# Performance work log

Hardware: AMD Instinct MI355X
Metric: run time of the kernel (lower is better)

## Reference

```python
import jax, jax.numpy as jnp
import numpy as np

TOP_K = 2
NUM_EXPERTS = 8
D_MODEL = 1024


def setup_inputs() -> dict:
    key = jax.random.key(0)
    kx, kw, kb = jax.random.split(key, 3)
    x = jax.random.normal(kx, (8, 4096, D_MODEL), dtype=jnp.float32)
    bound = 1.0 / np.sqrt(D_MODEL)
    W = jax.random.uniform(kw, (NUM_EXPERTS, D_MODEL), dtype=jnp.float32, minval=-bound, maxval=bound)
    b = jax.random.uniform(kb, (NUM_EXPERTS,), dtype=jnp.float32, minval=-bound, maxval=bound)
    return {"x": x, "W": W, "b": b}


def reference(x, W, b):
    # logits: [B, S, E]
    logits = jnp.einsum('bsd,ed->bse', x, W) + b
    values, indices = jax.lax.top_k(logits, TOP_K)  # [B,S,K]
    # softmax over a tensor that is -inf everywhere except top-k positions
    # == softmax over the top-k values, scattered back; non-selected experts get 0.
    topk_w = jax.nn.softmax(values, axis=-1)  # [B,S,K]
    one_hot = jax.nn.one_hot(indices, NUM_EXPERTS, dtype=logits.dtype)  # [B,S,K,E]
    weights = jnp.einsum('bsk,bske->bse', topk_w, one_hot)
    return weights, indices
```

## Files before the change

kernel.cpp:

```cpp
#include <hip/hip_runtime.h>
#include <math.h>

#define D_MODEL 1024
#define NUM_EXPERTS 8
#define TOP_K 2
#define TOKENS_PER_WAVE 4
#define WAVES_PER_BLOCK 4
#define TOKENS_PER_BLOCK (TOKENS_PER_WAVE * WAVES_PER_BLOCK)

__global__ __launch_bounds__(256) void gating_kernel(
    const float* __restrict__ x, const float* __restrict__ W,
    const float* __restrict__ b, float* __restrict__ out_w,
    float* __restrict__ out_idx, int n_tokens)
{
    __shared__ float Wlds[NUM_EXPERTS * D_MODEL];

    {
        const float4* Wg = (const float4*)W;
        float4* Ws = (float4*)Wlds;
        const int tid = threadIdx.x;
#pragma unroll
        for (int i = 0; i < (NUM_EXPERTS * D_MODEL / 4) / 256; ++i)
            Ws[tid + i * 256] = Wg[tid + i * 256];
    }
    __syncthreads();

    const int wave = threadIdx.x >> 6;
    const int lane = threadIdx.x & 63;
    const int token0 = (blockIdx.x * WAVES_PER_BLOCK + wave) * TOKENS_PER_WAVE;
    if (token0 >= n_tokens) return;

    float acc[TOKENS_PER_WAVE][NUM_EXPERTS];
#pragma unroll
    for (int t = 0; t < TOKENS_PER_WAVE; ++t)
#pragma unroll
        for (int e = 0; e < NUM_EXPERTS; ++e) acc[t][e] = 0.f;

#pragma unroll
    for (int j = 0; j < D_MODEL / 256; ++j) {
        float4 xv[TOKENS_PER_WAVE];
#pragma unroll
        for (int t = 0; t < TOKENS_PER_WAVE; ++t)
            xv[t] = *(const float4*)(x + (size_t)(token0 + t) * D_MODEL + j * 256 + lane * 4);
#pragma unroll
        for (int e = 0; e < NUM_EXPERTS; ++e) {
            float4 wv = *(const float4*)(Wlds + e * D_MODEL + j * 256 + lane * 4);
#pragma unroll
            for (int t = 0; t < TOKENS_PER_WAVE; ++t) {
                acc[t][e] += xv[t].x * wv.x + xv[t].y * wv.y +
                             xv[t].z * wv.z + xv[t].w * wv.w;
            }
        }
    }

#pragma unroll
    for (int t = 0; t < TOKENS_PER_WAVE; ++t)
#pragma unroll
        for (int e = 0; e < NUM_EXPERTS; ++e) {
            float v = acc[t][e];
#pragma unroll
            for (int s = 32; s >= 1; s >>= 1) v += __shfl_xor(v, s, 64);
            acc[t][e] = v;
        }

#pragma unroll
    for (int t = 0; t < TOKENS_PER_WAVE; ++t) {
        float v0 = -INFINITY, v1 = -INFINITY;
        int i0 = 0, i1 = 0;
#pragma unroll
        for (int e = 0; e < NUM_EXPERTS; ++e) {
            float v = acc[t][e] + b[e];
            if (v > v0) { v1 = v0; i1 = i0; v0 = v; i0 = e; }
            else if (v > v1) { v1 = v; i1 = e; }
        }
        float e1 = expf(v1 - v0);
        float w0 = 1.f / (1.f + e1);
        float w1 = e1 * w0;
        if (lane == t) {
            float wout[NUM_EXPERTS];
#pragma unroll
            for (int e = 0; e < NUM_EXPERTS; ++e)
                wout[e] = (e == i0) ? w0 : ((e == i1) ? w1 : 0.f);
            float4* dst = (float4*)(out_w + (size_t)(token0 + t) * NUM_EXPERTS);
            dst[0] = make_float4(wout[0], wout[1], wout[2], wout[3]);
            dst[1] = make_float4(wout[4], wout[5], wout[6], wout[7]);
            float2* di = (float2*)(out_idx + (size_t)(token0 + t) * TOP_K);
            *di = make_float2((float)i0, (float)i1);
        }
    }
}

extern "C" void kernel_launch(void* const* d_in, const int* in_sizes, int n_in,
                              void* d_out, int out_size, void* d_ws, size_t ws_size,
                              hipStream_t stream) {
    const float* x = (const float*)d_in[0];
    const float* W = (const float*)d_in[1];
    const float* b = (const float*)d_in[2];
    float* out = (float*)d_out;

    const int n_tokens = in_sizes[0] / D_MODEL;
    float* out_w   = out;
    float* out_idx = out + (size_t)n_tokens * NUM_EXPERTS;

    const int grid = (n_tokens + TOKENS_PER_BLOCK - 1) / TOKENS_PER_BLOCK;
    gating_kernel<<<grid, 256, 0, stream>>>(x, W, b, out_w, out_idx, n_tokens);
}
```

Before: 201.4 us.

## Map each token to an 8-lane group with short shuffle reductions

New measurement: 185.5 us. -7.9%, faster.

```diff
diff --git a/kernel.cpp b/kernel.cpp
--- a/kernel.cpp
+++ b/kernel.cpp
@@ -4,9 +4,12 @@
 #define D_MODEL 1024
 #define NUM_EXPERTS 8
 #define TOP_K 2
-#define TOKENS_PER_WAVE 4
+#define LANES_PER_TOKEN 8
+#define TOKENS_PER_WAVE 8
 #define WAVES_PER_BLOCK 4
 #define TOKENS_PER_BLOCK (TOKENS_PER_WAVE * WAVES_PER_BLOCK)
+
+typedef float f4 __attribute__((ext_vector_type(4)));
 
 __global__ __launch_bounds__(256) void gating_kernel(
     const float* __restrict__ x, const float* __restrict__ W,
@@ -16,8 +19,8 @@
     __shared__ float Wlds[NUM_EXPERTS * D_MODEL];
 
     {
-        const float4* Wg = (const float4*)W;
-        float4* Ws = (float4*)Wlds;
+        const f4* Wg = (const f4*)W;
+        f4* Ws = (f4*)Wlds;
         const int tid = threadIdx.x;
 #pragma unroll
         for (int i = 0; i < (NUM_EXPERTS * D_MODEL / 4) / 256; ++i)
@@ -27,66 +30,69 @@
 
     const int wave = threadIdx.x >> 6;
     const int lane = threadIdx.x & 63;
-    const int token0 = (blockIdx.x * WAVES_PER_BLOCK + wave) * TOKENS_PER_WAVE;
-    if (token0 >= n_tokens) return;
+    const int g = lane >> 3;
+    const int l = lane & 7;
+    const int token = blockIdx.x * TOKENS_PER_BLOCK + wave * TOKENS_PER_WAVE + g;
+    if (token >= n_tokens) return;
 
-    float acc[TOKENS_PER_WAVE][NUM_EXPERTS];
+    const f4* xg = (const f4*)x + (size_t)token * (D_MODEL / 4) + l;
+    const f4* Wl = (const f4*)Wlds + l;
+
+    float acc[NUM_EXPERTS];
 #pragma unroll
-    for (int t = 0; t < TOKENS_PER_WAVE; ++t)
-#pragma unroll
-        for (int e = 0; e < NUM_EXPERTS; ++e) acc[t][e] = 0.f;
+    for (int e = 0; e < NUM_EXPERTS; ++e) acc[e] = 0.f;
 
 #pragma unroll
-    for (int j = 0; j < D_MODEL / 256; ++j) {
-        float4 xv[TOKENS_PER_WAVE];
+    for (int c = 0; c < 4; ++c) {
+        f4 xa[8];
 #pragma unroll
-        for (int t = 0; t < TOKENS_PER_WAVE; ++t)
-            xv[t] = *(const float4*)(x + (size_t)(token0 + t) * D_MODEL + j * 256 + lane * 4);
+        for (int kk = 0; kk < 8; ++kk)
+            xa[kk] = __builtin_nontemporal_load(xg + (c * 8 + kk) * 8);
 #pragma unroll
         for (int e = 0; e < NUM_EXPERTS; ++e) {
-            float4 wv = *(const float4*)(Wlds + e * D_MODEL + j * 256 + lane * 4);
+            float s = acc[e];
 #pragma unroll
-            for (int t = 0; t < TOKENS_PER_WAVE; ++t) {
-                acc[t][e] += xv[t].x * wv.x + xv[t].y * wv.y +
-                             xv[t].z * wv.z + xv[t].w * wv.w;
+            for (int kk = 0; kk < 8; ++kk) {
+                const f4 wv = Wl[e * 256 + (c * 8 + kk) * 8];
+                s += xa[kk].x * wv.x + xa[kk].y * wv.y +
+                     xa[kk].z * wv.z + xa[kk].w * wv.w;
             }
+            acc[e] = s;
         }
     }
 
 #pragma unroll
-    for (int t = 0; t < TOKENS_PER_WAVE; ++t)
+    for (int e = 0; e < NUM_EXPERTS; ++e) {
+        float v = acc[e];
+        v += __shfl_xor(v, 1, 64);
+        v += __shfl_xor(v, 2, 64);
+        v += __shfl_xor(v, 4, 64);
+        acc[e] = v + b[e];
+    }
+
+    float v0 = -INFINITY, v1 = -INFINITY;
+    int i0 = 0, i1 = 0;
 #pragma unroll
-        for (int e = 0; e < NUM_EXPERTS; ++e) {
-            float v = acc[t][e];
-#pragma unroll
-            for (int s = 32; s >= 1; s >>= 1) v += __shfl_xor(v, s, 64);
-            acc[t][e] = v;
-        }
+    for (int e = 0; e < NUM_EXPERTS; ++e) {
+        float v = acc[e];
+        if (v > v0) { v1 = v0; i1 = i0; v0 = v; i0 = e; }
+        else if (v > v1) { v1 = v; i1 = e; }
+    }
+    const float e1 = expf(v1 - v0);
+    const float w0 = 1.f / (1.f + e1);
+    const float w1 = e1 * w0;
 
-#pragma unroll
-    for (int t = 0; t < TOKENS_PER_WAVE; ++t) {
-        float v0 = -INFINITY, v1 = -INFINITY;
-        int i0 = 0, i1 = 0;
-#pragma unroll
-        for (int e = 0; e < NUM_EXPERTS; ++e) {
-            float v = acc[t][e] + b[e];
-            if (v > v0) { v1 = v0; i1 = i0; v0 = v; i0 = e; }
-            else if (v > v1) { v1 = v; i1 = e; }
-        }
-        float e1 = expf(v1 - v0);
-        float w0 = 1.f / (1.f + e1);
-        float w1 = e1 * w0;
-        if (lane == t) {
-            float wout[NUM_EXPERTS];
-#pragma unroll
-            for (int e = 0; e < NUM_EXPERTS; ++e)
-                wout[e] = (e == i0) ? w0 : ((e == i1) ? w1 : 0.f);
-            float4* dst = (float4*)(out_w + (size_t)(token0 + t) * NUM_EXPERTS);
-            dst[0] = make_float4(wout[0], wout[1], wout[2], wout[3]);
-            dst[1] = make_float4(wout[4], wout[5], wout[6], wout[7]);
-            float2* di = (float2*)(out_idx + (size_t)(token0 + t) * TOP_K);
-            *di = make_float2((float)i0, (float)i1);
-        }
+    if (l < 2) {
+        const int base = l * 4;
+        f4 v4;
+        v4.x = (base + 0 == i0) ? w0 : ((base + 0 == i1) ? w1 : 0.f);
+        v4.y = (base + 1 == i0) ? w0 : ((base + 1 == i1) ? w1 : 0.f);
+        v4.z = (base + 2 == i0) ? w0 : ((base + 2 == i1) ? w1 : 0.f);
+        v4.w = (base + 3 == i0) ? w0 : ((base + 3 == i1) ? w1 : 0.f);
+        ((f4*)(out_w + (size_t)token * NUM_EXPERTS))[l] = v4;
+    } else if (l == 2) {
+        *(float2*)(out_idx + (size_t)token * TOP_K) =
+            make_float2((float)i0, (float)i1);
     }
 }
 
```
